# Optimization experiments

Hardware: AMD Instinct MI355X
Metric: run time of the kernel (lower is better)

Reference implementation:

```python
import jax, jax.numpy as jnp
import numpy as np

TAU = 0.5
EPS = 1e-6
RAY_STEPS = 128
N_SECANT = 8
STEPS_IN = 64
STEPS_OUT = 32
RADIUS = 1.0
ADA_START, ADA_END, ADA_DECAY = 2.0, 0.1, 1.5e-5
IT = 100000
DEPTH_NEAR = 0.0
DELTA = float(max(ADA_START * np.exp(-ADA_DECAY * IT), ADA_END))


def _occ_val(p, W1, b1, W2, b2):
    # occupancy probability minus tau (sign change = surface crossing)
    h = jax.nn.softplus(p @ W1 + b1)
    return jax.nn.sigmoid((h @ W2 + b2)[..., 0]) - TAU


def _rgb_alpha(p, v, W1, b1, W2, b2, Wc1, bc1, Wc2, bc2):
    alpha = _occ_val(p, W1, b1, W2, b2) + TAU
    f = jax.nn.relu(jnp.concatenate([p, v], -1) @ Wc1 + bc1)
    rgb = jax.nn.sigmoid(f @ Wc2 + bc2)
    return rgb, alpha


def _forward(pixels, camera_mat, world_mat, scale_mat, W1, b1, W2, b2, Wc1, bc1, Wc2, bc2):
    B, N, _ = pixels.shape
    # transform_to_world with all matrices inverted: p_world = S^-1 W^-1 C^-1 p_hom
    M = jnp.linalg.inv(scale_mat) @ jnp.linalg.inv(world_mat) @ jnp.linalg.inv(camera_mat)
    ones = jnp.ones((B, N, 1), pixels.dtype)
    p_h = jnp.concatenate([pixels, ones, ones], -1)  # (x, y, 1, 1) with depth 1
    pixels_world = jnp.einsum('bij,bnj->bni', M, p_h)[..., :3]
    origin = jnp.array([0.0, 0.0, 0.0, 1.0], pixels.dtype)
    cam0 = jnp.einsum('bij,j->bi', M, origin)[..., :3]                 # (B,3)
    camera_world = jnp.broadcast_to(cam0[:, None, :], (B, N, 3))
    ray = pixels_world - camera_world
    ray = ray / jnp.linalg.norm(ray, axis=-1, keepdims=True)

    # ---- sphere intersection ----
    rcd = jnp.einsum('bnd,bd->bn', ray, cam0)
    under = rcd ** 2 - (jnp.sum(cam0 ** 2, -1)[:, None] - RADIUS ** 2)
    mask_int = under > 0
    s = jnp.sqrt(jnp.where(mask_int, under, 1.0))                      # safe sqrt
    inters = jnp.stack([-s - rcd, s - rcd], -1)
    inters = jnp.where(mask_int[..., None], inters, 0.0)
    inters = jnp.maximum(inters, 0.0)                                  # (B,N,2)
    d_far = inters[..., 1]

    # ---- ray marching + secant root finding (no grad in original) ----
    t = jnp.linspace(0.0, 1.0, RAY_STEPS, dtype=pixels.dtype)
    d_prop = d_far[..., None] * t                                      # (B,N,S)
    p_prop = camera_world[:, :, None, :] + ray[:, :, None, :] * d_prop[..., None]
    val = _occ_val(p_prop, W1, b1, W2, b2)                             # (B,N,S)
    mask_0_free = val[..., 0] < 0
    sign = jnp.sign(val[..., :-1] * val[..., 1:])
    sign = jnp.concatenate([sign, jnp.ones_like(sign[..., :1])], -1)
    cost = sign * jnp.arange(RAY_STEPS, 0, -1, dtype=pixels.dtype)
    ind = jnp.argmin(cost, -1)
    mask_sc = jnp.min(cost, -1) < 0
    f_low = jnp.take_along_axis(val, ind[..., None], -1)[..., 0]
    mask = mask_sc & (f_low < 0) & mask_int & mask_0_free
    ind_hi = jnp.minimum(ind + 1, RAY_STEPS - 1)
    d_low = jnp.take_along_axis(d_prop, ind[..., None], -1)[..., 0]
    d_high = jnp.take_along_axis(d_prop, ind_hi[..., None], -1)[..., 0]
    f_high = jnp.take_along_axis(val, ind_hi[..., None], -1)[..., 0]

    def sec(f_l, f_h, d_l, d_h):
        den = f_h - f_l
        return jnp.where(jnp.abs(den) > 1e-12, -f_l * (d_h - d_l) / den + d_l, 0.5 * (d_l + d_h))

    def body(i, c):
        d_p, d_l, f_l, d_h, f_h = c
        f_m = _occ_val(camera_world + ray * d_p[..., None], W1, b1, W2, b2)
        low = f_m < 0
        d_l = jnp.where(low, d_p, d_l); f_l = jnp.where(low, f_m, f_l)
        d_h = jnp.where(low, d_h, d_p); f_h = jnp.where(low, f_h, f_m)
        return (sec(f_l, f_h, d_l, d_h), d_l, f_l, d_h, f_h)

    d_pred0 = sec(f_low, f_high, d_low, d_high)
    d_pred, _, _, _, _ = jax.lax.fori_loop(0, N_SECANT, body, (d_pred0, d_low, f_low, d_high, f_high))
    d_i = jnp.where(mask, d_pred, jnp.inf)
    d_i = jnp.where(mask_0_free, d_i, 0.0)
    d_i = jax.lax.stop_gradient(d_i)

    # ---- depth interval selection ----
    mask_zero = d_i == 0
    mask_pred = jnp.isfinite(d_i)
    dists = jnp.where(mask_pred, d_i, 1.0)
    dists = jnp.where(mask_zero, 0.0, dists)[0]                        # batch 1, as original
    obj_mask = (mask_pred & ~mask_zero)[0]                             # (N,)
    cam_f = camera_world.reshape(-1, 3)
    ray_f = ray.reshape(-1, 3)
    d_surf = inters.reshape(-1, 2)[:, 1]
    dnp = jnp.maximum(dists - DELTA, DEPTH_NEAR)
    dfp = jnp.minimum(dists + DELTA, d_surf)
    FULL = STEPS_IN + STEPS_OUT
    t_full = jnp.linspace(0.0, 1.0, FULL, dtype=pixels.dtype)
    d_bg = d_surf[:, None] * t_full                                    # depth_range[0] = 0
    t_in = jnp.linspace(0.0, 1.0, STEPS_IN, dtype=pixels.dtype)
    t_out = jnp.linspace(0.0, 1.0, STEPS_OUT, dtype=pixels.dtype)
    d_in = dnp[:, None] * (1.0 - t_in) + dfp[:, None] * t_in
    d_out = dnp[:, None] * t_out
    d_obj = jnp.sort(jnp.concatenate([d_out, d_in], -1), -1)
    d_all = jnp.where(obj_mask[:, None], d_obj, d_bg)                  # (N, FULL)

    # ---- shading + alpha compositing ----
    p_fg = cam_f[:, None, :] + ray_f[:, None, :] * d_all[..., None]    # (N,FULL,3)
    v_fg = jnp.broadcast_to(-ray_f[:, None, :], p_fg.shape)
    rgb, alpha = _rgb_alpha(p_fg, v_fg, W1, b1, W2, b2, Wc1, bc1, Wc2, bc2)
    trans = jnp.cumprod(jnp.concatenate([jnp.ones_like(alpha[:, :1]), 1.0 - alpha + EPS], -1), -1)[:, :-1]
    w = alpha * trans
    rgb_values = jnp.sum(w[..., None] * rgb, -2)
    return rgb_values.reshape(B, N, 3)


def setup_inputs() -> dict:
    key = jax.random.key(0)
    ks = jax.random.split(key, 8)
    B, N, H = 1, 4096, 128
    pixels = jax.random.uniform(ks[0], (B, N, 2), minval=-1.0, maxval=1.0, dtype=jnp.float32)
    camera_mat = jnp.broadcast_to(jnp.diag(jnp.array([2.0, 2.0, 1.0, 1.0], jnp.float32)), (B, 4, 4))
    world_mat = jnp.broadcast_to(jnp.array([[1, 0, 0, 0], [0, 1, 0, 0], [0, 0, 1, 2.0], [0, 0, 0, 1]], jnp.float32), (B, 4, 4))
    scale_mat = jnp.broadcast_to(jnp.eye(4, dtype=jnp.float32), (B, 4, 4))
    W1 = jax.random.normal(ks[1], (3, H), jnp.float32)
    b1 = 0.1 * jax.random.normal(ks[2], (H,), jnp.float32)
    W2 = 0.5 * jax.random.normal(ks[3], (H, 1), jnp.float32)
    b2 = jnp.zeros((1,), jnp.float32)
    Wc1 = 0.5 * jax.random.normal(ks[4], (6, H), jnp.float32)
    bc1 = jnp.zeros((H,), jnp.float32)
    Wc2 = 0.5 * jax.random.normal(ks[5], (H, 3), jnp.float32)
    bc2 = jnp.zeros((3,), jnp.float32)
    return dict(pixels=pixels, camera_mat=camera_mat, world_mat=world_mat, scale_mat=scale_mat,
                W1=W1, b1=b1, W2=W2, b2=b2, Wc1=Wc1, bc1=bc1, Wc2=Wc2, bc2=bc2)


def reference(pixels, camera_mat, world_mat, scale_mat, W1, b1, W2, b2, Wc1, bc1, Wc2, bc2):
    return _forward(pixels, camera_mat, world_mat, scale_mat, W1, b1, W2, b2, Wc1, bc1, Wc2, bc2)
```

## Files before the change

kernel.cpp:

```cpp
#include <hip/hip_runtime.h>
#include <math.h>


namespace {

constexpr int H_    = 128;
constexpr int RS    = 128;
constexpr int NSEC  = 8;
constexpr int SOUT_ = 32;
constexpr int SIN_  = 64;
constexpr int FULL_ = 96;
constexpr float EPSA   = 1e-6f;
constexpr float DELTA_ = 0.44626032029685964f;
constexpr float L2E    = 1.4426950408889634f;
constexpr float LN2    = 0.6931471805599453f;

typedef __attribute__((ext_vector_type(2))) float f2;

__device__ __forceinline__ f2 s2(float v) { return f2{v, v}; }

constexpr float PC0 =  0.5849625007211562f;
constexpr float PC1 =  0.4808983469629878f;
constexpr float PC2 = -0.0801497244938313f;
constexpr float PC3 =  0.0178110498875181f;
constexpr float PC4 = -0.0044527624718795f;
constexpr float PC5 =  0.0011873633258345f;
constexpr float PC6 = -0.0003298231460651f;

__device__ __forceinline__ f2 sp2p(f2 u) {
    f2 e;
    e.x = __builtin_amdgcn_exp2f(-fabsf(u.x));
    e.y = __builtin_amdgcn_exp2f(-fabsf(u.y));
    f2 t  = e + e - 1.0f;
    f2 t2 = t * t;
    f2 t4 = t2 * t2;
    f2 A = __builtin_elementwise_fma(t, s2(PC1), s2(PC0));
    f2 B = __builtin_elementwise_fma(t, s2(PC3), s2(PC2));
    f2 C = __builtin_elementwise_fma(t, s2(PC5), s2(PC4));
    f2 E = __builtin_elementwise_fma(t2, B, A);
    f2 F = __builtin_elementwise_fma(t2, s2(PC6), C);
    f2 p = __builtin_elementwise_fma(t4, F, E);
    return __builtin_elementwise_max(u, s2(0.0f)) + p;
}

__device__ __forceinline__ float sigmoid_fast(float x) {
    return __builtin_amdgcn_rcpf(1.0f + __expf(-x));
}
__device__ __forceinline__ float sgnf(float p) {
    return (p > 0.0f) ? 1.0f : ((p < 0.0f) ? -1.0f : 0.0f);
}
__device__ __forceinline__ float secant_step(float f_l, float f_h, float d_l, float d_h) {
    float den = f_h - f_l;
    if (fabsf(den) > 1e-12f) return -f_l * (d_h - d_l) / den + d_l;
    return 0.5f * (d_l + d_h);
}
__device__ __forceinline__ float2 ld2(const float* p) {
    return *reinterpret_cast<const float2*>(p);
}

__device__ void inv4(const float* m, float* o) {
    float inv[16];
    inv[0]  =  m[5]*m[10]*m[15] - m[5]*m[11]*m[14] - m[9]*m[6]*m[15] + m[9]*m[7]*m[14] + m[13]*m[6]*m[11] - m[13]*m[7]*m[10];
    inv[4]  = -m[4]*m[10]*m[15] + m[4]*m[11]*m[14] + m[8]*m[6]*m[15] - m[8]*m[7]*m[14] - m[12]*m[6]*m[11] + m[12]*m[7]*m[10];
    inv[8]  =  m[4]*m[9]*m[15]  - m[4]*m[11]*m[13] - m[8]*m[5]*m[15] + m[8]*m[7]*m[13] + m[12]*m[5]*m[11] - m[12]*m[7]*m[9];
    inv[12] = -m[4]*m[9]*m[14]  + m[4]*m[10]*m[13] + m[8]*m[5]*m[14] - m[8]*m[6]*m[13] - m[12]*m[5]*m[10] + m[12]*m[6]*m[9];
    inv[1]  = -m[1]*m[10]*m[15] + m[1]*m[11]*m[14] + m[9]*m[2]*m[15] - m[9]*m[3]*m[14] - m[13]*m[2]*m[11] + m[13]*m[3]*m[10];
    inv[5]  =  m[0]*m[10]*m[15] - m[0]*m[11]*m[14] - m[8]*m[2]*m[15] + m[8]*m[3]*m[14] + m[12]*m[2]*m[11] - m[12]*m[3]*m[10];
    inv[9]  = -m[0]*m[9]*m[15]  + m[0]*m[11]*m[13] + m[8]*m[1]*m[15] - m[8]*m[3]*m[13] - m[12]*m[1]*m[11] + m[12]*m[3]*m[9];
    inv[13] =  m[0]*m[9]*m[14]  - m[0]*m[10]*m[13] - m[8]*m[1]*m[14] + m[8]*m[2]*m[13] + m[12]*m[1]*m[10] - m[12]*m[2]*m[9];
    inv[2]  =  m[1]*m[6]*m[15]  - m[1]*m[7]*m[14]  - m[5]*m[2]*m[15] + m[5]*m[3]*m[14] + m[13]*m[2]*m[7]  - m[13]*m[3]*m[6];
    inv[6]  = -m[0]*m[6]*m[15]  + m[0]*m[7]*m[14]  + m[4]*m[2]*m[15] - m[4]*m[3]*m[14] - m[12]*m[2]*m[7]  + m[12]*m[3]*m[6];
    inv[10] =  m[0]*m[5]*m[15]  - m[0]*m[7]*m[13]  - m[4]*m[1]*m[15] + m[4]*m[3]*m[13] + m[12]*m[1]*m[7]  - m[12]*m[3]*m[5];
    inv[14] = -m[0]*m[5]*m[14]  + m[0]*m[6]*m[13]  + m[4]*m[1]*m[14] - m[4]*m[2]*m[13] - m[12]*m[1]*m[6]  + m[12]*m[2]*m[5];
    inv[3]  = -m[1]*m[6]*m[11]  + m[1]*m[7]*m[10]  + m[5]*m[2]*m[11] - m[5]*m[3]*m[10] - m[9]*m[2]*m[7]   + m[9]*m[3]*m[6];
    inv[7]  =  m[0]*m[6]*m[11]  - m[0]*m[7]*m[10]  - m[4]*m[2]*m[11] + m[4]*m[3]*m[10] + m[8]*m[2]*m[7]   - m[8]*m[3]*m[6];
    inv[11] = -m[0]*m[5]*m[11]  + m[0]*m[7]*m[9]   + m[4]*m[1]*m[11] - m[4]*m[3]*m[9]  - m[8]*m[1]*m[7]   + m[8]*m[3]*m[5];
    inv[15] =  m[0]*m[5]*m[10]  - m[0]*m[6]*m[9]   - m[4]*m[1]*m[10] + m[4]*m[2]*m[9]  + m[8]*m[1]*m[6]   - m[8]*m[2]*m[5];
    float det = m[0]*inv[0] + m[1]*inv[4] + m[2]*inv[8] + m[3]*inv[12];
    float idet = 1.0f / det;
    for (int i = 0; i < 16; i++) o[i] = inv[i] * idet;
}

__global__ __launch_bounds__(64) void render_k(
    const float* __restrict__ pixels,
    const float* __restrict__ Cm, const float* __restrict__ Wm, const float* __restrict__ Sm,
    const float* __restrict__ W1, const float* __restrict__ b1,
    const float* __restrict__ W2, const float* __restrict__ b2,
    const float* __restrict__ Wc1, const float* __restrict__ bc1,
    const float* __restrict__ Wc2, const float* __restrict__ bc2,
    float* __restrict__ out, int N)
{
    const int lane = threadIdx.x;
    const int r    = blockIdx.x;

    __shared__ float4 sP0[H_/2];
    __shared__ float4 sP1[H_/2];
    __shared__ float4 sP2[H_/2];
    __shared__ float4 sP3[H_/2];
    __shared__ f2     sW2[H_/2];
    __shared__ float  sInv[3][16];
    __shared__ float  sT[16], sM[16];
    __shared__ float  sPad[16];

    const int u0 = 2 * lane;
    const float2 w1xv = ld2(W1 + u0);
    const float2 w1yv = ld2(W1 + H_ + u0);
    const float2 w1zv = ld2(W1 + 2*H_ + u0);
    const float2 b1v  = ld2(b1 + u0);
    const float2 w2v  = ld2(W2 + u0);
    const float2 q0v  = ld2(Wc1 + u0);
    const float2 q1v  = ld2(Wc1 + H_ + u0);
    const float2 q2v  = ld2(Wc1 + 2*H_ + u0);
    const float2 q3v  = ld2(Wc1 + 3*H_ + u0);
    const float2 q4v  = ld2(Wc1 + 4*H_ + u0);
    const float2 q5v  = ld2(Wc1 + 5*H_ + u0);
    const float2 bc1v = ld2(bc1 + u0);
    const float2 wc2a = ld2(Wc2 + 3*u0);
    const float2 wc2b = ld2(Wc2 + 3*u0 + 2);
    const float2 wc2c = ld2(Wc2 + 3*u0 + 4);
    const float b2v  = b2[0];
    const float bc20 = bc2[0], bc21 = bc2[1], bc22 = bc2[2];

    {
        const float* mm = (lane == 0) ? Cm : ((lane == 1) ? Wm : Sm);
        float o[16];
        inv4(mm, o);
        if (lane < 3)
            for (int k = 0; k < 16; k++) sInv[lane][k] = o[k];
    }
    __syncthreads();
    if (lane < 16) {
        int row = lane >> 2, col = lane & 3;
        float s = 0.0f;
        for (int k = 0; k < 4; k++) s += sInv[1][row*4 + k] * sInv[0][k*4 + col];
        sT[lane] = s;
    }
    __syncthreads();
    if (lane < 16) {
        int row = lane >> 2, col = lane & 3;
        float s = 0.0f;
        for (int k = 0; k < 4; k++) s += sInv[2][row*4 + k] * sT[k*4 + col];
        sM[lane] = s;
    }
    __syncthreads();

    float cx, cy, cz, rx, ry, rz, dfar;
    int mint;
    {
        const float px_ = pixels[2*r], py_ = pixels[2*r + 1];
        float cam[3], dir[3];
        for (int i = 0; i < 3; i++) {
            cam[i] = sM[4*i + 3];
            float pw = sM[4*i + 0]*px_ + sM[4*i + 1]*py_ + sM[4*i + 2] + sM[4*i + 3];
            dir[i] = pw - cam[i];
        }
        float nrm = sqrtf(dir[0]*dir[0] + dir[1]*dir[1] + dir[2]*dir[2]);
        rx = dir[0]/nrm; ry = dir[1]/nrm; rz = dir[2]/nrm;
        cx = cam[0]; cy = cam[1]; cz = cam[2];
        float rcd = rx*cx + ry*cy + rz*cz;
        float cc  = cx*cx + cy*cy + cz*cz;
        float under = rcd*rcd - (cc - 1.0f);
        mint = under > 0.0f;
        float s = sqrtf(mint ? under : 1.0f);
        dfar = mint ? fmaxf(s - rcd, 0.0f) : 0.0f;
    }

    float a2k[2], c2k[2], w2k[2];
    float cCr[2], w0r[2], w1r[2], w2r[2];
    {
        a2k[0] = (w1xv.x*rx + w1yv.x*ry + w1zv.x*rz) * L2E;
        a2k[1] = (w1xv.y*rx + w1yv.y*ry + w1zv.y*rz) * L2E;
        c2k[0] = (w1xv.x*cx + w1yv.x*cy + w1zv.x*cz + b1v.x) * L2E;
        c2k[1] = (w1xv.y*cx + w1yv.y*cy + w1zv.y*cz + b1v.y) * L2E;
        w2k[0] = w2v.x * LN2;
        w2k[1] = w2v.y * LN2;
        float aC0 = q0v.x*rx + q1v.x*ry + q2v.x*rz;
        float aC1 = q0v.y*rx + q1v.y*ry + q2v.y*rz;
        cCr[0] = q0v.x*cx + q1v.x*cy + q2v.x*cz + bc1v.x - (q3v.x*rx + q4v.x*ry + q5v.x*rz);
        cCr[1] = q0v.y*cx + q1v.y*cy + q2v.y*cz + bc1v.y - (q3v.y*rx + q4v.y*ry + q5v.y*rz);
        w0r[0] = wc2a.x; w1r[0] = wc2a.y; w2r[0] = wc2b.x;
        w0r[1] = wc2b.y; w1r[1] = wc2c.x; w2r[1] = wc2c.y;
        sP0[lane] = float4{a2k[0], a2k[1], c2k[0], c2k[1]};
        sP1[lane] = float4{w2k[0], w2k[1], aC0, aC1};
        sP2[lane] = float4{cCr[0], cCr[1], w0r[0], w0r[1]};
        sP3[lane] = float4{w1r[0], w1r[1], w2r[0], w2r[1]};
        sW2[lane] = f2{w2k[0], w2k[1]};
        if (lane < 16) sPad[lane] = 0.0f;
    }
    __syncthreads();

    float alpha0, r0c, g0c, b0c;
    float alpha1, r1c, g1c, b1c;

    if (dfar == 0.0f) {
        f2 sp = sp2p(f2{c2k[0], c2k[1]});
        float part = sp.x*w2k[0] + sp.y*w2k[1];
        f2 ff = __builtin_elementwise_max(f2{cCr[0], cCr[1]}, s2(0.0f));
        float A0 = ff.x*w0r[0] + ff.y*w0r[1];
        float A1 = ff.x*w1r[0] + ff.y*w1r[1];
        float A2 = ff.x*w2r[0] + ff.y*w2r[1];
#pragma unroll
        for (int off = 32; off; off >>= 1) {
            part += __shfl_xor(part, off, 64);
            A0   += __shfl_xor(A0,   off, 64);
            A1   += __shfl_xor(A1,   off, 64);
            A2   += __shfl_xor(A2,   off, 64);
        }
        alpha0 = sigmoid_fast(part + b2v);
        r0c = sigmoid_fast(A0 + bc20);
        g0c = sigmoid_fast(A1 + bc21);
        b0c = sigmoid_fast(A2 + bc22);
        alpha1 = alpha0; r1c = r0c; g1c = g0c; b1c = b0c;
    } else {
        const float inv127 = 1.0f / (RS - 1);

        float l0;
        {
            f2 sp = sp2p(f2{c2k[0], c2k[1]});
            float part = sp.x*w2k[0] + sp.y*w2k[1];
#pragma unroll
            for (int off = 32; off; off >>= 1) part += __shfl_xor(part, off, 64);
            l0 = part + b2v;
        }

        float d_i;
        if (l0 >= 0.0f) {
            d_i = 0.0f;
        } else {
            auto march_logit = [&](float dsmp) -> float {
                const f2 dd = s2(dsmp);
                f2 acc0 = s2(0.0f), acc1 = s2(0.0f);
                float4 nb[4]; f2 nw[4];
#pragma unroll
                for (int k = 0; k < 4; ++k) { nb[k] = sP0[k]; nw[k] = sW2[k]; }
                for (int g = 0; g < H_/8; ++g) {
                    float4 cb[4]; f2 cw[4];
#pragma unroll
                    for (int k = 0; k < 4; ++k) { cb[k] = nb[k]; cw[k] = nw[k]; }
                    const int base = (g + 1) * 4;
#pragma unroll
                    for (int k = 0; k < 4; ++k) { nb[k] = sP0[base + k]; nw[k] = sW2[base + k]; }
#pragma unroll
                    for (int k = 0; k < 4; ++k) {
                        f2 u = __builtin_elementwise_fma(f2{cb[k].x, cb[k].y}, dd,
                                                         f2{cb[k].z, cb[k].w});
                        f2 s = sp2p(u);
                        if (k & 1) acc1 = __builtin_elementwise_fma(s, cw[k], acc1);
                        else       acc0 = __builtin_elementwise_fma(s, cw[k], acc0);
                    }
                }
                f2 acc = acc0 + acc1;
                return acc.x + acc.y + b2v;
            };

            float lA = march_logit(dfar * ((float)lane * inv127));
            float lan = __shfl_down(lA, 1, 64);
            float ca = (lane < 63) ? sgnf(lA * lan) * (float)(RS - lane) : 1.0f;
            float cmin = ca; int ind = lane;
#pragma unroll
            for (int off = 32; off; off >>= 1) {
                float c2 = __shfl_xor(cmin, off, 64);
                int   i2 = __shfl_xor(ind,  off, 64);
                if (c2 < cmin || (c2 == cmin && i2 < ind)) { cmin = c2; ind = i2; }
            }
            int crossed = cmin < 0.0f;
            float ll = 0.0f, lh = 0.0f;
            if (crossed) {
                ll = __shfl(lA, ind, 64);
                lh = __shfl(lA, ind + 1, 64);
            } else {
                float lB = march_logit(dfar * ((float)(lane + 64) * inv127));
                float l63 = __shfl(lA, 63, 64);
                float l64 = __shfl(lB, 0, 64);
                if (l63 * l64 < 0.0f) {
                    crossed = 1; ind = 63;
                    ll = l63; lh = l64;
                } else {
                    float lbn = __shfl_down(lB, 1, 64);
                    float cb = (lane < 63) ? sgnf(lB * lbn) * (float)(64 - lane) : 1.0f;
                    float cminb = cb; int indl = lane;
#pragma unroll
                    for (int off = 32; off; off >>= 1) {
                        float c2 = __shfl_xor(cminb, off, 64);
                        int   i2 = __shfl_xor(indl,  off, 64);
                        if (c2 < cminb || (c2 == cminb && i2 < indl)) { cminb = c2; indl = i2; }
                    }
                    if (cminb < 0.0f) {
                        crossed = 1; ind = 64 + indl;
                        ll = __shfl(lB, indl, 64);
                        lh = __shfl(lB, indl + 1, 64);
                    }
                }
            }

            const int msk = crossed && (ll < 0.0f) && mint;
            if (msk) {
                float f_low  = sigmoid_fast(ll) - 0.5f;
                float f_high = sigmoid_fast(lh) - 0.5f;
                float d_l = dfar * ((float)ind * inv127);
                float d_h = dfar * ((float)(ind + 1) * inv127);
                float f_l = f_low, f_h = f_high;
                float d_p = secant_step(f_l, f_h, d_l, d_h);
                for (int it = 0; it < NSEC; it++) {
                    f2 u2 = __builtin_elementwise_fma(f2{a2k[0], a2k[1]}, s2(d_p),
                                                      f2{c2k[0], c2k[1]});
                    f2 sp = sp2p(u2);
                    float part = sp.x*w2k[0] + sp.y*w2k[1];
#pragma unroll
                    for (int off = 32; off; off >>= 1) part += __shfl_xor(part, off, 64);
                    float fm = sigmoid_fast(part + b2v) - 0.5f;
                    bool low = fm < 0.0f;
                    d_l = low ? d_p : d_l;  f_l = low ? fm : f_l;
                    d_h = low ? d_h : d_p;  f_h = low ? f_h : fm;
                    d_p = secant_step(f_l, f_h, d_l, d_h);
                }
                d_i = d_p;
            } else {
                d_i = INFINITY;
            }
        }

        const int mask_zero = (d_i == 0.0f);
        const int mask_pred = isfinite(d_i);
        float dists = mask_pred ? d_i : 1.0f;
        if (mask_zero) dists = 0.0f;
        const int obj = mask_pred && !mask_zero;
        const float dnp = fmaxf(dists - DELTA_, 0.0f);
        const float dfp = fminf(dists + DELTA_, dfar);

        auto sample_d = [&](int s) -> float {
            if (obj) {
                if (s < SOUT_) return dnp * ((float)s * (1.0f / (SOUT_ - 1)));
                float u = (float)(s - SOUT_) * (1.0f / (SIN_ - 1));
                return dnp * (1.0f - u) + dfp * u;
            }
            return dfar * ((float)s * (1.0f / (FULL_ - 1)));
        };

        auto shade = [&](int jb, int cnt, float dsmp,
                         float& SOo, float& A0o, float& A1o, float& A2o) {
            const f2 dd = s2(dsmp);
            f2 SO = s2(0.0f), A0 = s2(0.0f), A1 = s2(0.0f), A2 = s2(0.0f);
            float4 n0[2], n1[2], n2[2], n3[2];
#pragma unroll
            for (int k = 0; k < 2; ++k) {
                n0[k] = sP0[jb + k]; n1[k] = sP1[jb + k];
                n2[k] = sP2[jb + k]; n3[k] = sP3[jb + k];
            }
            for (int g = 0; g < cnt/2; ++g) {
                float4 c0[2], c1[2], c2q[2], c3[2];
#pragma unroll
                for (int k = 0; k < 2; ++k) {
                    c0[k] = n0[k]; c1[k] = n1[k]; c2q[k] = n2[k]; c3[k] = n3[k];
                }
                const int base = jb + (g + 1) * 2;
#pragma unroll
                for (int k = 0; k < 2; ++k) {
                    n0[k] = sP0[base + k]; n1[k] = sP1[base + k];
                    n2[k] = sP2[base + k]; n3[k] = sP3[base + k];
                }
#pragma unroll
                for (int k = 0; k < 2; ++k) {
                    f2 u = __builtin_elementwise_fma(f2{c0[k].x, c0[k].y}, dd,
                                                     f2{c0[k].z, c0[k].w});
                    SO = __builtin_elementwise_fma(sp2p(u), f2{c1[k].x, c1[k].y}, SO);
                    f2 f = __builtin_elementwise_max(
                               __builtin_elementwise_fma(f2{c1[k].z, c1[k].w}, dd,
                                                         f2{c2q[k].x, c2q[k].y}),
                               s2(0.0f));
                    A0 = __builtin_elementwise_fma(f, f2{c2q[k].z, c2q[k].w}, A0);
                    A1 = __builtin_elementwise_fma(f, f2{c3[k].x, c3[k].y}, A1);
                    A2 = __builtin_elementwise_fma(f, f2{c3[k].z, c3[k].w}, A2);
                }
            }
            SOo = SO.x + SO.y; A0o = A0.x + A0.y;
            A1o = A1.x + A1.y; A2o = A2.x + A2.y;
        };

        {
            float SOs, A0s, A1s, A2s;
            shade(0, H_/2, sample_d(lane), SOs, A0s, A1s, A2s);
            alpha0 = sigmoid_fast(SOs + b2v);
            r0c = sigmoid_fast(A0s + bc20);
            g0c = sigmoid_fast(A1s + bc21);
            b0c = sigmoid_fast(A2s + bc22);
        }

        {
            const int s1 = 64 + (lane & 31);
            const int jb = (lane >> 5) * (H_/4);
            float SOs, A0s, A1s, A2s;
            shade(jb, H_/4, sample_d(s1), SOs, A0s, A1s, A2s);
            SOs += __shfl_xor(SOs, 32, 64);
            A0s += __shfl_xor(A0s, 32, 64);
            A1s += __shfl_xor(A1s, 32, 64);
            A2s += __shfl_xor(A2s, 32, 64);
            alpha1 = sigmoid_fast(SOs + b2v);
            r1c = sigmoid_fast(A0s + bc20);
            g1c = sigmoid_fast(A1s + bc21);
            b1c = sigmoid_fast(A2s + bc22);
        }
    }

    {
        float mA = 1.0f - alpha0 + EPSA;
        float p = mA;
#pragma unroll
        for (int off = 1; off < 64; off <<= 1) {
            float v = __shfl_up(p, off, 64);
            if (lane >= off) p *= v;
        }
        float TexA = __shfl_up(p, 1, 64);
        if (lane == 0) TexA = 1.0f;
        float TA = __shfl(p, 63, 64);
        float wA = alpha0 * TexA;

        float mB = (lane < 32) ? (1.0f - alpha1 + EPSA) : 1.0f;
        float pb = mB;
#pragma unroll
        for (int off = 1; off < 32; off <<= 1) {
            float v = __shfl_up(pb, off, 64);
            if (lane >= off) pb *= v;
        }
        float TexB = __shfl_up(pb, 1, 64);
        if (lane == 0) TexB = 1.0f;
        float wB = (lane < 32) ? alpha1 * TexB * TA : 0.0f;

        float s0 = wA*r0c + wB*r1c;
        float s1 = wA*g0c + wB*g1c;
        float s2v = wA*b0c + wB*b1c;
#pragma unroll
        for (int off = 32; off; off >>= 1) {
            s0  += __shfl_xor(s0,  off, 64);
            s1  += __shfl_xor(s1,  off, 64);
            s2v += __shfl_xor(s2v, off, 64);
        }
        if (lane == 0) {
            out[3*r + 0] = s0;
            out[3*r + 1] = s1;
            out[3*r + 2] = s2v;
        }
    }
}

}

extern "C" void kernel_launch(void* const* d_in, const int* in_sizes, int n_in,
                              void* d_out, int out_size, void* d_ws, size_t ws_size,
                              hipStream_t stream) {
    const float* pixels = (const float*)d_in[0];
    const float* Cm  = (const float*)d_in[1];
    const float* Wm  = (const float*)d_in[2];
    const float* Sm  = (const float*)d_in[3];
    const float* W1  = (const float*)d_in[4];
    const float* b1  = (const float*)d_in[5];
    const float* W2  = (const float*)d_in[6];
    const float* b2  = (const float*)d_in[7];
    const float* Wc1 = (const float*)d_in[8];
    const float* bc1 = (const float*)d_in[9];
    const float* Wc2 = (const float*)d_in[10];
    const float* bc2 = (const float*)d_in[11];
    float* out = (float*)d_out;

    const int N = in_sizes[0] / 2;
    hipLaunchKernelGGL(render_k, dim3(N), dim3(64), 0, stream,
                       pixels, Cm, Wm, Sm, W1, b1, W2, b2, Wc1, bc1, Wc2, bc2, out, N);
}
```

Baseline: 105.7 us.

## Shrink shared tables, read output weights from global, pack two samples per lane in shading

Reduces LDS staging from five arrays to two (sP0 and a new sC). W2 and Wc2 are now read directly from global memory through cached pointers, with the LN2 scale applied once after the reduction. The shading phase now evaluates both sample sets in one pass, each lane's two samples placed in the halves of a packed f2 over all hidden units. This replaces the split half-hidden pass and its cross-lane shuffle. It cuts LDS footprint and the shuffle work, but may add global-load latency inside the hot loops and duplicates the scalar hidden-unit work across both samples.

```diff
diff --git a/kernel.cpp b/kernel.cpp
--- a/kernel.cpp
+++ b/kernel.cpp
@@ -94,32 +94,12 @@
     const int r    = blockIdx.x;
 
     __shared__ float4 sP0[H_/2];
-    __shared__ float4 sP1[H_/2];
-    __shared__ float4 sP2[H_/2];
-    __shared__ float4 sP3[H_/2];
-    __shared__ f2     sW2[H_/2];
+    __shared__ float4 sC [H_/2];
     __shared__ float  sInv[3][16];
     __shared__ float  sT[16], sM[16];
-    __shared__ float  sPad[16];
-
-    const int u0 = 2 * lane;
-    const float2 w1xv = ld2(W1 + u0);
-    const float2 w1yv = ld2(W1 + H_ + u0);
-    const float2 w1zv = ld2(W1 + 2*H_ + u0);
-    const float2 b1v  = ld2(b1 + u0);
-    const float2 w2v  = ld2(W2 + u0);
-    const float2 q0v  = ld2(Wc1 + u0);
-    const float2 q1v  = ld2(Wc1 + H_ + u0);
-    const float2 q2v  = ld2(Wc1 + 2*H_ + u0);
-    const float2 q3v  = ld2(Wc1 + 3*H_ + u0);
-    const float2 q4v  = ld2(Wc1 + 4*H_ + u0);
-    const float2 q5v  = ld2(Wc1 + 5*H_ + u0);
-    const float2 bc1v = ld2(bc1 + u0);
-    const float2 wc2a = ld2(Wc2 + 3*u0);
-    const float2 wc2b = ld2(Wc2 + 3*u0 + 2);
-    const float2 wc2c = ld2(Wc2 + 3*u0 + 4);
-    const float b2v  = b2[0];
-    const float bc20 = bc2[0], bc21 = bc2[1], bc22 = bc2[2];
+
+    const float2* __restrict__ W2p  = reinterpret_cast<const float2*>(W2);
+    const float2* __restrict__ Wc2p = reinterpret_cast<const float2*>(Wc2);
 
     {
         const float* mm = (lane == 0) ? Cm : ((lane == 1) ? Wm : Sm);
@@ -165,28 +145,42 @@
         dfar = mint ? fmaxf(s - rcd, 0.0f) : 0.0f;
     }
 
+    const int u0 = 2 * lane;
     float a2k[2], c2k[2], w2k[2];
     float cCr[2], w0r[2], w1r[2], w2r[2];
     {
+        const float2 w1xv = ld2(W1 + u0);
+        const float2 w1yv = ld2(W1 + H_ + u0);
+        const float2 w1zv = ld2(W1 + 2*H_ + u0);
+        const float2 b1v  = ld2(b1 + u0);
+        const float2 w2v  = ld2(W2 + u0);
         a2k[0] = (w1xv.x*rx + w1yv.x*ry + w1zv.x*rz) * L2E;
         a2k[1] = (w1xv.y*rx + w1yv.y*ry + w1zv.y*rz) * L2E;
         c2k[0] = (w1xv.x*cx + w1yv.x*cy + w1zv.x*cz + b1v.x) * L2E;
         c2k[1] = (w1xv.y*cx + w1yv.y*cy + w1zv.y*cz + b1v.y) * L2E;
         w2k[0] = w2v.x * LN2;
         w2k[1] = w2v.y * LN2;
+        const float2 q0v  = ld2(Wc1 + u0);
+        const float2 q1v  = ld2(Wc1 + H_ + u0);
+        const float2 q2v  = ld2(Wc1 + 2*H_ + u0);
+        const float2 q3v  = ld2(Wc1 + 3*H_ + u0);
+        const float2 q4v  = ld2(Wc1 + 4*H_ + u0);
+        const float2 q5v  = ld2(Wc1 + 5*H_ + u0);
+        const float2 bc1v = ld2(bc1 + u0);
         float aC0 = q0v.x*rx + q1v.x*ry + q2v.x*rz;
         float aC1 = q0v.y*rx + q1v.y*ry + q2v.y*rz;
         cCr[0] = q0v.x*cx + q1v.x*cy + q2v.x*cz + bc1v.x - (q3v.x*rx + q4v.x*ry + q5v.x*rz);
         cCr[1] = q0v.y*cx + q1v.y*cy + q2v.y*cz + bc1v.y - (q3v.y*rx + q4v.y*ry + q5v.y*rz);
+        const float2 wc2a = ld2(Wc2 + 3*u0);
+        const float2 wc2b = ld2(Wc2 + 3*u0 + 2);
+        const float2 wc2c = ld2(Wc2 + 3*u0 + 4);
         w0r[0] = wc2a.x; w1r[0] = wc2a.y; w2r[0] = wc2b.x;
         w0r[1] = wc2b.y; w1r[1] = wc2c.x; w2r[1] = wc2c.y;
         sP0[lane] = float4{a2k[0], a2k[1], c2k[0], c2k[1]};
-        sP1[lane] = float4{w2k[0], w2k[1], aC0, aC1};
-        sP2[lane] = float4{cCr[0], cCr[1], w0r[0], w0r[1]};
-        sP3[lane] = float4{w1r[0], w1r[1], w2r[0], w2r[1]};
-        sW2[lane] = f2{w2k[0], w2k[1]};
-        if (lane < 16) sPad[lane] = 0.0f;
-    }
+        sC [lane] = float4{aC0,    aC1,    cCr[0], cCr[1]};
+    }
+    const float b2v  = b2[0];
+    const float bc20 = bc2[0], bc21 = bc2[1], bc22 = bc2[2];
     __syncthreads();
 
     float alpha0, r0c, g0c, b0c;
@@ -229,28 +223,15 @@
         } else {
             auto march_logit = [&](float dsmp) -> float {
                 const f2 dd = s2(dsmp);
-                f2 acc0 = s2(0.0f), acc1 = s2(0.0f);
-                float4 nb[4]; f2 nw[4];
-#pragma unroll
-                for (int k = 0; k < 4; ++k) { nb[k] = sP0[k]; nw[k] = sW2[k]; }
-                for (int g = 0; g < H_/8; ++g) {
-                    float4 cb[4]; f2 cw[4];
-#pragma unroll
-                    for (int k = 0; k < 4; ++k) { cb[k] = nb[k]; cw[k] = nw[k]; }
-                    const int base = (g + 1) * 4;
-#pragma unroll
-                    for (int k = 0; k < 4; ++k) { nb[k] = sP0[base + k]; nw[k] = sW2[base + k]; }
-#pragma unroll
-                    for (int k = 0; k < 4; ++k) {
-                        f2 u = __builtin_elementwise_fma(f2{cb[k].x, cb[k].y}, dd,
-                                                         f2{cb[k].z, cb[k].w});
-                        f2 s = sp2p(u);
-                        if (k & 1) acc1 = __builtin_elementwise_fma(s, cw[k], acc1);
-                        else       acc0 = __builtin_elementwise_fma(s, cw[k], acc0);
-                    }
+                f2 acc = s2(0.0f);
+#pragma unroll 4
+                for (int j = 0; j < H_/2; ++j) {
+                    float4 q0 = sP0[j];
+                    float2 wv = W2p[j];
+                    f2 u = __builtin_elementwise_fma(f2{q0.x, q0.y}, dd, f2{q0.z, q0.w});
+                    acc = __builtin_elementwise_fma(sp2p(u), f2{wv.x, wv.y}, acc);
                 }
-                f2 acc = acc0 + acc1;
-                return acc.x + acc.y + b2v;
+                return LN2 * (acc.x + acc.y) + b2v;
             };
 
             float lA = march_logit(dfar * ((float)lane * inv127));
@@ -295,11 +276,10 @@
 
             const int msk = crossed && (ll < 0.0f) && mint;
             if (msk) {
-                float f_low  = sigmoid_fast(ll) - 0.5f;
-                float f_high = sigmoid_fast(lh) - 0.5f;
+                float f_l = sigmoid_fast(ll) - 0.5f;
+                float f_h = sigmoid_fast(lh) - 0.5f;
                 float d_l = dfar * ((float)ind * inv127);
                 float d_h = dfar * ((float)(ind + 1) * inv127);
-                float f_l = f_low, f_h = f_high;
                 float d_p = secant_step(f_l, f_h, d_l, d_h);
                 for (int it = 0; it < NSEC; it++) {
                     f2 u2 = __builtin_elementwise_fma(f2{a2k[0], a2k[1]}, s2(d_p),
@@ -337,68 +317,40 @@
             return dfar * ((float)s * (1.0f / (FULL_ - 1)));
         };
 
-        auto shade = [&](int jb, int cnt, float dsmp,
-                         float& SOo, float& A0o, float& A1o, float& A2o) {
-            const f2 dd = s2(dsmp);
+        {
+            const f2 dd = f2{sample_d(lane), sample_d(64 + (lane & 31))};
             f2 SO = s2(0.0f), A0 = s2(0.0f), A1 = s2(0.0f), A2 = s2(0.0f);
-            float4 n0[2], n1[2], n2[2], n3[2];
-#pragma unroll
-            for (int k = 0; k < 2; ++k) {
-                n0[k] = sP0[jb + k]; n1[k] = sP1[jb + k];
-                n2[k] = sP2[jb + k]; n3[k] = sP3[jb + k];
+#pragma unroll 4
+            for (int j = 0; j < H_/2; ++j) {
+                float4 q = sP0[j];
+                float4 c = sC[j];
+                float2 wv = W2p[j];
+                float2 wa = Wc2p[3*j];
+                float2 wb = Wc2p[3*j + 1];
+                float2 wc = Wc2p[3*j + 2];
+                f2 u0f = __builtin_elementwise_fma(s2(q.x), dd, s2(q.z));
+                SO = __builtin_elementwise_fma(sp2p(u0f), s2(wv.x), SO);
+                f2 f0 = __builtin_elementwise_max(
+                            __builtin_elementwise_fma(s2(c.x), dd, s2(c.z)), s2(0.0f));
+                A0 = __builtin_elementwise_fma(f0, s2(wa.x), A0);
+                A1 = __builtin_elementwise_fma(f0, s2(wa.y), A1);
+                A2 = __builtin_elementwise_fma(f0, s2(wb.x), A2);
+                f2 u1f = __builtin_elementwise_fma(s2(q.y), dd, s2(q.w));
+                SO = __builtin_elementwise_fma(sp2p(u1f), s2(wv.y), SO);
+                f2 f1 = __builtin_elementwise_max(
+                            __builtin_elementwise_fma(s2(c.y), dd, s2(c.w)), s2(0.0f));
+                A0 = __builtin_elementwise_fma(f1, s2(wb.y), A0);
+                A1 = __builtin_elementwise_fma(f1, s2(wc.x), A1);
+                A2 = __builtin_elementwise_fma(f1, s2(wc.y), A2);
             }
-            for (int g = 0; g < cnt/2; ++g) {
-                float4 c0[2], c1[2], c2q[2], c3[2];
-#pragma unroll
-                for (int k = 0; k < 2; ++k) {
-                    c0[k] = n0[k]; c1[k] = n1[k]; c2q[k] = n2[k]; c3[k] = n3[k];
-                }
-                const int base = jb + (g + 1) * 2;
-#pragma unroll
-                for (int k = 0; k < 2; ++k) {
-                    n0[k] = sP0[base + k]; n1[k] = sP1[base + k];
-                    n2[k] = sP2[base + k]; n3[k] = sP3[base + k];
-                }
-#pragma unroll
-                for (int k = 0; k < 2; ++k) {
-                    f2 u = __builtin_elementwise_fma(f2{c0[k].x, c0[k].y}, dd,
-                                                     f2{c0[k].z, c0[k].w});
-                    SO = __builtin_elementwise_fma(sp2p(u), f2{c1[k].x, c1[k].y}, SO);
-                    f2 f = __builtin_elementwise_max(
-                               __builtin_elementwise_fma(f2{c1[k].z, c1[k].w}, dd,
-                                                         f2{c2q[k].x, c2q[k].y}),
-                               s2(0.0f));
-                    A0 = __builtin_elementwise_fma(f, f2{c2q[k].z, c2q[k].w}, A0);
-                    A1 = __builtin_elementwise_fma(f, f2{c3[k].x, c3[k].y}, A1);
-                    A2 = __builtin_elementwise_fma(f, f2{c3[k].z, c3[k].w}, A2);
-                }
-            }
-            SOo = SO.x + SO.y; A0o = A0.x + A0.y;
-            A1o = A1.x + A1.y; A2o = A2.x + A2.y;
-        };
-
-        {
-            float SOs, A0s, A1s, A2s;
-            shade(0, H_/2, sample_d(lane), SOs, A0s, A1s, A2s);
-            alpha0 = sigmoid_fast(SOs + b2v);
-            r0c = sigmoid_fast(A0s + bc20);
-            g0c = sigmoid_fast(A1s + bc21);
-            b0c = sigmoid_fast(A2s + bc22);
-        }
-
-        {
-            const int s1 = 64 + (lane & 31);
-            const int jb = (lane >> 5) * (H_/4);
-            float SOs, A0s, A1s, A2s;
-            shade(jb, H_/4, sample_d(s1), SOs, A0s, A1s, A2s);
-            SOs += __shfl_xor(SOs, 32, 64);
-            A0s += __shfl_xor(A0s, 32, 64);
-            A1s += __shfl_xor(A1s, 32, 64);
-            A2s += __shfl_xor(A2s, 32, 64);
-            alpha1 = sigmoid_fast(SOs + b2v);
-            r1c = sigmoid_fast(A0s + bc20);
-            g1c = sigmoid_fast(A1s + bc21);
-            b1c = sigmoid_fast(A2s + bc22);
+            alpha0 = sigmoid_fast(LN2 * SO.x + b2v);
+            r0c = sigmoid_fast(A0.x + bc20);
+            g0c = sigmoid_fast(A1.x + bc21);
+            b0c = sigmoid_fast(A2.x + bc22);
+            alpha1 = sigmoid_fast(LN2 * SO.y + b2v);
+            r1c = sigmoid_fast(A0.y + bc20);
+            g1c = sigmoid_fast(A1.y + bc21);
+            b1c = sigmoid_fast(A2.y + bc22);
         }
     }
 
```

New measurement: 104.6 us. Within noise of the previous version (-1.0%).
